# Optimization experiments

Measured on AMD Instinct MI355X. Metric: run time of the kernel, lower is better.

The kernel has to match this reference:

```python
import jax, jax.numpy as jnp
import numpy as np

N_NODES = 20000
N_EDGES = 320000
F_IN, HID, OUT = 128, 256, 32
N_LAYERS = 30
N_GRAPHS = 16


def setup_inputs() -> dict:
    key = jax.random.key(0)
    ks = jax.random.split(key, 10)
    x = jax.random.normal(ks[0], (N_NODES, F_IN), dtype=jnp.float32)
    edge_list = jax.random.randint(ks[1], (2, N_EDGES), 0, N_NODES, dtype=jnp.int64)
    batch = jnp.sort(jax.random.randint(ks[2], (N_NODES,), 0, N_GRAPHS, dtype=jnp.int64))
    # GCNConv weights: conv1, 29 middle layers, final linear
    W1 = jax.random.normal(ks[3], (F_IN, HID), dtype=jnp.float32) / np.sqrt(F_IN)
    b1 = jnp.zeros((HID,), dtype=jnp.float32)
    Wm = jax.random.normal(ks[4], (N_LAYERS - 1, HID, HID), dtype=jnp.float32) / np.sqrt(HID)
    bm = jnp.zeros((N_LAYERS - 1, HID), dtype=jnp.float32)
    Wlin = jax.random.normal(ks[5], (HID, OUT), dtype=jnp.float32) / np.sqrt(HID)
    blin = jnp.zeros((OUT,), dtype=jnp.float32)
    return {"x": x, "edge_list": edge_list, "batch": batch,
            "W1": W1, "b1": b1, "Wm": Wm, "bm": bm, "Wlin": Wlin, "blin": blin}


def reference(x, edge_list, batch, W1, b1, Wm, bm, Wlin, blin):
    n = x.shape[0]
    loop = jnp.arange(n, dtype=edge_list.dtype)
    src = jnp.concatenate([edge_list[0], loop])  # senders (+ self loops)
    dst = jnp.concatenate([edge_list[1], loop])  # receivers (+ self loops)
    # symmetric GCN normalization: deg counted at receivers incl. self loops
    deg = jax.ops.segment_sum(jnp.ones_like(dst, dtype=x.dtype), dst, num_segments=n)
    dinv = jnp.where(deg > 0, jax.lax.rsqrt(deg), 0.0)
    norm = dinv[src] * dinv[dst]  # [E+n]

    def conv(h, W, b):
        h = h @ W  # dense linear first (PyG GCNConv)
        agg = jax.ops.segment_sum(h[src] * norm[:, None], dst, num_segments=n)
        return jax.nn.relu(agg + b)

    h = conv(x, W1, b1)

    def step(h, wb):
        W, b = wb
        return conv(h, W, b), None

    h, _ = jax.lax.scan(step, h, (Wm, bm))

    # global mean pool over graphs
    counts = jax.ops.segment_sum(jnp.ones((n,), x.dtype), batch, num_segments=N_GRAPHS)
    pooled = jax.ops.segment_sum(h, batch, num_segments=N_GRAPHS) / jnp.maximum(counts, 1.0)[:, None]
    return pooled @ Wlin + blin
```

## Files before the change

kernel.cpp:

```cpp
#include <hip/hip_runtime.h>

typedef unsigned short u16;
typedef unsigned int u32;
typedef __attribute__((ext_vector_type(8))) _Float16 f16x8;
typedef __attribute__((ext_vector_type(4))) float f32x4;
typedef __attribute__((ext_vector_type(8))) u16 u16x8;

#define N_NODES 20000
#define N_EDGES 320000
#define F_IN 128
#define HID 256
#define OUT_F 32
#define N_LAYERS 30
#define N_GRAPHS 16
#define ELLCAP 64

__device__ __forceinline__ float h2f(u16 u) {
    _Float16 h;
    __builtin_memcpy(&h, &u, 2);
    return (float)h;
}
__device__ __forceinline__ u16 f2h(float f) {
    _Float16 h = (_Float16)f;
    u16 u;
    __builtin_memcpy(&u, &h, 2);
    return u;
}

__device__ __forceinline__ void gl_lds16(const u16* g, u16* l) {
    __builtin_amdgcn_global_load_lds((const u32*)g, (u32*)l, 16, 0, 0);
}

__global__ void fill_ell_kernel(const int* __restrict__ src, const int* __restrict__ dst,
                                int* __restrict__ cursor, u16* __restrict__ ell_col, int E) {
    int e = blockIdx.x * blockDim.x + threadIdx.x;
    if (e >= E) return;
    int s = src[e], d = dst[e];
    int slot = atomicAdd(&cursor[d], 1);
    if (slot < ELLCAP) ell_col[d * ELLCAP + slot] = (u16)s;
}

__global__ void dinv_kernel(const int* __restrict__ cnt, float* __restrict__ dinv, int n) {
    int i = blockIdx.x * blockDim.x + threadIdx.x;
    if (i < n) dinv[i] = rsqrtf((float)(cnt[i] + 1));
}

__global__ void prescale_x_kernel(const float* __restrict__ x, const int* __restrict__ cnt,
                                  u16* __restrict__ xs, int total) {
    int i = blockIdx.x * 256 + threadIdx.x;
    if (i < total) xs[i] = f2h(x[i] * rsqrtf((float)(cnt[i >> 7] + 1)));
}

__global__ __launch_bounds__(256) void transpose_f16_tiled(const float* __restrict__ W,
                                                           u16* __restrict__ T,
                                                           int K, int N) {
    __shared__ float tile[32][33];
    const int l = blockIdx.y;
    const int ntn = N >> 5;
    const int kt = blockIdx.x / ntn, ntile = blockIdx.x % ntn;
    const float* Wl = W + (size_t)l * K * N;
    u16* Tl = T + (size_t)l * K * N;
    const int r8 = threadIdx.x >> 5, c = threadIdx.x & 31;
    #pragma unroll
    for (int rr = 0; rr < 4; ++rr) {
        int r = rr * 8 + r8;
        tile[r][c] = Wl[(size_t)(kt * 32 + r) * N + ntile * 32 + c];
    }
    __syncthreads();
    #pragma unroll
    for (int rr = 0; rr < 4; ++rr) {
        int n = rr * 8 + r8;
        float v = tile[c][n];
        Tl[(size_t)(ntile * 32 + n) * K + kt * 32 + c] = f2h(v);
    }
}

template <int K>
__global__ __launch_bounds__(256, 3) void layer_fused(const u16* __restrict__ hs,
                                                      const u16* __restrict__ B,
                                                      const u16* __restrict__ ell_col,
                                                      const int* __restrict__ cnt,
                                                      const float* __restrict__ dinv,
                                                      const float* __restrict__ bias,
                                                      const float* __restrict__ rowscale,
                                                      u16* __restrict__ Ch,
                                                      float* __restrict__ C) {
    __shared__ u16 cols[32 * ELLCAP];
    __shared__ __align__(16) u16 gs[32 * HID];
    __shared__ __align__(16) u16 Bs[256 * 64];
    const int node0 = blockIdx.x * 32;
    const int tid = threadIdx.x;
    *(u16x8*)&cols[tid * 8] = *(const u16x8*)&ell_col[(size_t)node0 * ELLCAP + tid * 8];
    const int nd = tid >> 3, sub = tid & 7;
    const int node = node0 + nd;
    int c = cnt[node]; c = c < ELLCAP ? c : ELLCAP;
    const float dd = dinv[node];
    __syncthreads();
    const u16* cl = &cols[nd * ELLCAP];
    const int nb = (c + 7) >> 3;
    constexpr int S = K / 64;
    const int p0 = blockIdx.x & (S - 1);

    #pragma unroll 1
    for (int pi = 0; pi < S; ++pi) {
        const int p = (pi + p0) & (S - 1);
        const int f = p * 64 + sub * 8;
        f32x4 a0 = {}, a1 = {};
        {
            u16x8 sv = *(const u16x8*)(hs + (size_t)node * K + f);
            #pragma unroll
            for (int i = 0; i < 4; ++i) a0[i] += h2f(sv[i]);
            #pragma unroll
            for (int i = 0; i < 4; ++i) a1[i] += h2f(sv[i + 4]);
        }
        if (nb > 0) {
            u16x8 vbuf[8];
            u16x8 cc = *(const u16x8*)&cl[0];
            #pragma unroll
            for (int j = 0; j < 8; ++j) vbuf[j] = *(const u16x8*)(hs + (size_t)cc[j] * K + f);
            int base = 0;
            for (int b = 1; b < nb; ++b) {
                u16x8 cn = *(const u16x8*)&cl[b * 8];
                u16x8 vn[8];
                #pragma unroll
                for (int j = 0; j < 8; ++j) vn[j] = *(const u16x8*)(hs + (size_t)cn[j] * K + f);
                #pragma unroll
                for (int j = 0; j < 8; ++j) {
                    #pragma unroll
                    for (int i = 0; i < 4; ++i) a0[i] += h2f(vbuf[j][i]);
                    #pragma unroll
                    for (int i = 0; i < 4; ++i) a1[i] += h2f(vbuf[j][i + 4]);
                }
                base += 8;
                #pragma unroll
                for (int j = 0; j < 8; ++j) vbuf[j] = vn[j];
            }
            const u16x8 zz = {};
            #pragma unroll
            for (int j = 0; j < 8; ++j) {
                u16x8 v = (base + j < c) ? vbuf[j] : zz;
                #pragma unroll
                for (int i = 0; i < 4; ++i) a0[i] += h2f(v[i]);
                #pragma unroll
                for (int i = 0; i < 4; ++i) a1[i] += h2f(v[i + 4]);
            }
        }
        u16x8 o;
        #pragma unroll
        for (int i = 0; i < 4; ++i) o[i] = f2h(a0[i] * dd);
        #pragma unroll
        for (int i = 0; i < 4; ++i) o[i + 4] = f2h(a1[i] * dd);
        const int cc_ = p * 8 + sub;
        *(u16x8*)&gs[nd * K + ((cc_ ^ (nd & 7)) << 3)] = o;
    }

    const int wave = tid >> 6, lane = tid & 63;
    const int lr = lane >> 3, lc = lane & 7;
    #pragma unroll
    for (int q = 0; q < 8; ++q) {
        int rl = (wave * 8 + q) * 8 + lr;
        gl_lds16(B + (size_t)rl * K + ((lc ^ (rl & 7)) << 3), &Bs[(wave * 8 + q) * 512]);
    }
    f32x4 acc[2][4] = {};
    #pragma unroll
    for (int k = 0; k < S; ++k) {
        __syncthreads();
        const int k0 = k * 64;
        #pragma unroll
        for (int kk = 0; kk < 2; ++kk) {
            const int c8 = kk * 4 + (lane >> 4);
            f16x8 bf[4];
            #pragma unroll
            for (int nt = 0; nt < 4; ++nt) {
                int n = wave * 64 + nt * 16 + (lane & 15);
                bf[nt] = *(const f16x8*)&Bs[n * 64 + ((c8 ^ (n & 7)) << 3)];
            }
            #pragma unroll
            for (int mt = 0; mt < 2; ++mt) {
                int ml = mt * 16 + (lane & 15);
                int cg = (k0 >> 3) + c8;
                f16x8 af = *(const f16x8*)&gs[ml * K + ((cg ^ (ml & 7)) << 3)];
                #pragma unroll
                for (int nt = 0; nt < 4; ++nt)
                    acc[mt][nt] = __builtin_amdgcn_mfma_f32_16x16x32_f16(af, bf[nt], acc[mt][nt], 0, 0, 0);
            }
        }
        if (k + 1 < S) {
            __syncthreads();
            const int kn = k0 + 64;
            #pragma unroll
            for (int q = 0; q < 8; ++q) {
                int rl = (wave * 8 + q) * 8 + lr;
                gl_lds16(B + (size_t)rl * K + kn + ((lc ^ (rl & 7)) << 3), &Bs[(wave * 8 + q) * 512]);
            }
        }
    }
    __syncthreads();
    if (Ch) {
        #pragma unroll
        for (int mt = 0; mt < 2; ++mt) {
            #pragma unroll
            for (int r = 0; r < 4; ++r) {
                int lrow = mt * 16 + ((lane >> 4) << 2) + r;
                float sc = rowscale ? rowscale[node0 + lrow] : 1.f;
                #pragma unroll
                for (int nt = 0; nt < 4; ++nt) {
                    int gc = wave * 64 + nt * 16 + (lane & 15);
                    float v = sc * fmaxf(acc[mt][nt][r] + bias[gc], 0.f);
                    gs[lrow * HID + (gc ^ ((lrow & 7) << 3))] = f2h(v);
                }
            }
        }
        __syncthreads();
        const int row = tid >> 3, colb = (tid & 7) * 32;
        #pragma unroll
        for (int j = 0; j < 4; ++j) {
            int cs = (colb + j * 8) ^ ((row & 7) << 3);
            *(u16x8*)(Ch + (size_t)(node0 + row) * HID + colb + j * 8) = *(const u16x8*)&gs[row * HID + cs];
        }
    } else {
        float* Bf = (float*)Bs;
        #pragma unroll
        for (int mt = 0; mt < 2; ++mt) {
            #pragma unroll
            for (int r = 0; r < 4; ++r) {
                int lrow = mt * 16 + ((lane >> 4) << 2) + r;
                float sc = rowscale ? rowscale[node0 + lrow] : 1.f;
                #pragma unroll
                for (int nt = 0; nt < 4; ++nt) {
                    int gc = wave * 64 + nt * 16 + (lane & 15);
                    float v = sc * fmaxf(acc[mt][nt][r] + bias[gc], 0.f);
                    Bf[lrow * HID + (gc ^ ((lrow & 7) << 2))] = v;
                }
            }
        }
        __syncthreads();
        const int row = tid >> 3, colb = (tid & 7) * 32;
        #pragma unroll
        for (int j = 0; j < 8; ++j) {
            int cs = (colb + j * 4) ^ ((row & 7) << 2);
            *(f32x4*)(C + (size_t)(node0 + row) * HID + colb + j * 4) = *(const f32x4*)&Bf[row * HID + cs];
        }
    }
}

#define POOL_CHUNK 32
__global__ __launch_bounds__(256) void pool_kernel(const float* __restrict__ h,
                                                   const int* __restrict__ batch,
                                                   float* __restrict__ pool_sum) {
    int f = threadIdx.x;
    int start = blockIdx.x * POOL_CHUNK;
    int end = start + POOL_CHUNK; end = end < N_NODES ? end : N_NODES;
    if (start >= N_NODES) return;
    int gcur = batch[start];
    float acc = 0.f;
    for (int i = start; i < end; ++i) {
        int g = batch[i];
        if (g != gcur) { atomicAdd(&pool_sum[gcur * HID + f], acc); acc = 0.f; gcur = g; }
        acc += h[(size_t)i * HID + f];
    }
    atomicAdd(&pool_sum[gcur * HID + f], acc);
}

__device__ int lb_int(const int* __restrict__ a, int n, int v) {
    int lo = 0, hi = n;
    while (lo < hi) {
        int mid = (lo + hi) >> 1;
        if (a[mid] < v) lo = mid + 1; else hi = mid;
    }
    return lo;
}

__global__ void final_linear_kernel(const float* __restrict__ pool_sum,
                                    const int* __restrict__ batch,
                                    const float* __restrict__ Wlin,
                                    const float* __restrict__ blin,
                                    float* __restrict__ out) {
    int idx = blockIdx.x * blockDim.x + threadIdx.x;
    if (idx >= N_GRAPHS * OUT_F) return;
    int g = idx / OUT_F, o = idx % OUT_F;
    int lo = lb_int(batch, N_NODES, g);
    int hi = lb_int(batch, N_NODES, g + 1);
    float cinv = 1.f / fmaxf((float)(hi - lo), 1.f);
    float s = blin[o];
    for (int k = 0; k < HID; ++k) s += (pool_sum[g * HID + k] * cinv) * Wlin[k * OUT_F + o];
    out[idx] = s;
}

static inline size_t align_up(size_t x, size_t a) { return (x + a - 1) & ~(a - 1); }

extern "C" void kernel_launch(void* const* d_in, const int* in_sizes, int n_in,
                              void* d_out, int out_size, void* d_ws, size_t ws_size,
                              hipStream_t stream) {
    const float* x     = (const float*)d_in[0];
    const int*   elist = (const int*)d_in[1];
    const int*   batch = (const int*)d_in[2];
    const float* W1    = (const float*)d_in[3];
    const float* b1    = (const float*)d_in[4];
    const float* Wm    = (const float*)d_in[5];
    const float* bm    = (const float*)d_in[6];
    const float* Wlin  = (const float*)d_in[7];
    const float* blin  = (const float*)d_in[8];
    float* outp = (float*)d_out;

    const int* srcA = elist;
    const int* dstA = elist + N_EDGES;

    char* ws = (char*)d_ws;
    size_t off = 0;
    float* h      = (float*)(ws + off); off = align_up(off + sizeof(float) * N_NODES * HID, 1024);
    u16*   hA     = (u16*)(ws + off);   off = align_up(off + sizeof(u16) * N_NODES * HID, 1024);
    u16*   hB     = (u16*)(ws + off);   off = align_up(off + sizeof(u16) * N_NODES * HID, 1024);
    u16*   xs     = (u16*)(ws + off);   off = align_up(off + sizeof(u16) * N_NODES * F_IN, 1024);
    u16*   W1T    = (u16*)(ws + off);   off = align_up(off + sizeof(u16) * F_IN * HID, 1024);
    u16*   WmT    = (u16*)(ws + off);   off = align_up(off + sizeof(u16) * (N_LAYERS - 1) * HID * HID, 1024);
    int*   cursor = (int*)(ws + off);   off = align_up(off + sizeof(int) * N_NODES, 1024);
    float* dinv   = (float*)(ws + off); off = align_up(off + sizeof(float) * N_NODES, 1024);
    u16*   ell_col = (u16*)(ws + off);  off = align_up(off + sizeof(u16) * N_NODES * ELLCAP, 1024);
    float* pool_sum = (float*)(ws + off); off = align_up(off + sizeof(float) * N_GRAPHS * HID, 1024);

    hipMemsetAsync(cursor, 0, sizeof(int) * N_NODES, stream);
    hipMemsetAsync(ell_col, 0, sizeof(u16) * N_NODES * ELLCAP, stream);
    hipMemsetAsync(pool_sum, 0, sizeof(float) * N_GRAPHS * HID, stream);

    fill_ell_kernel<<<(N_EDGES + 255) / 256, 256, 0, stream>>>(srcA, dstA, cursor, ell_col, N_EDGES);
    dinv_kernel<<<(N_NODES + 255) / 256, 256, 0, stream>>>(cursor, dinv, N_NODES);
    prescale_x_kernel<<<(N_NODES * F_IN + 255) / 256, 256, 0, stream>>>(x, cursor, xs, N_NODES * F_IN);

    transpose_f16_tiled<<<dim3((F_IN / 32) * (HID / 32), 1), 256, 0, stream>>>(W1, W1T, F_IN, HID);
    transpose_f16_tiled<<<dim3((HID / 32) * (HID / 32), N_LAYERS - 1), 256, 0, stream>>>(Wm, WmT, HID, HID);

    const int lgrid = N_NODES / 32;
    layer_fused<F_IN><<<lgrid, 256, 0, stream>>>(xs, W1T, ell_col, cursor, dinv, b1, dinv, hA, h);
    u16* cur = hA; u16* nxt = hB;
    for (int l = 0; l < N_LAYERS - 1; ++l) {
        const bool last = (l == N_LAYERS - 2);
        layer_fused<HID><<<lgrid, 256, 0, stream>>>(cur, WmT + (size_t)l * HID * HID,
                                                    ell_col, cursor, dinv,
                                                    bm + (size_t)l * HID,
                                                    last ? nullptr : dinv,
                                                    last ? nullptr : nxt, h);
        u16* t = cur; cur = nxt; nxt = t;
    }
    pool_kernel<<<(N_NODES + POOL_CHUNK - 1) / POOL_CHUNK, 256, 0, stream>>>(h, batch, pool_sum);
    final_linear_kernel<<<2, 256, 0, stream>>>(pool_sum, batch, Wlin, blin, outp);
}
```

Before: 948.1 us.

## Read weight fragments directly from global memory instead of staging in LDS

Drops the LDS staging buffer for the weight matrix B and loads MFMA B-fragments straight from global memory, which is expected to hit L2 since every block reads the same weights. This removes the per-k-step barriers and the async global-to-LDS copies, and frees 32KB of LDS per block so more blocks can be resident. The fp32 output path also writes accumulators directly to global instead of transposing through LDS. The cost is uncoalesced 16-byte global reads repeated per block and scattered scalar fp32 stores.

```diff
diff --git a/kernel.cpp b/kernel.cpp
--- a/kernel.cpp
+++ b/kernel.cpp
@@ -25,10 +25,6 @@
     u16 u;
     __builtin_memcpy(&u, &h, 2);
     return u;
-}
-
-__device__ __forceinline__ void gl_lds16(const u16* g, u16* l) {
-    __builtin_amdgcn_global_load_lds((const u32*)g, (u32*)l, 16, 0, 0);
 }
 
 __global__ void fill_ell_kernel(const int* __restrict__ src, const int* __restrict__ dst,
@@ -87,7 +83,6 @@
                                                       float* __restrict__ C) {
     __shared__ u16 cols[32 * ELLCAP];
     __shared__ __align__(16) u16 gs[32 * HID];
-    __shared__ __align__(16) u16 Bs[256 * 64];
     const int node0 = blockIdx.x * 32;
     const int tid = threadIdx.x;
     *(u16x8*)&cols[tid * 8] = *(const u16x8*)&ell_col[(size_t)node0 * ELLCAP + tid * 8];
@@ -155,16 +150,10 @@
     }
 
     const int wave = tid >> 6, lane = tid & 63;
-    const int lr = lane >> 3, lc = lane & 7;
-    #pragma unroll
-    for (int q = 0; q < 8; ++q) {
-        int rl = (wave * 8 + q) * 8 + lr;
-        gl_lds16(B + (size_t)rl * K + ((lc ^ (rl & 7)) << 3), &Bs[(wave * 8 + q) * 512]);
-    }
     f32x4 acc[2][4] = {};
+    __syncthreads();
     #pragma unroll
     for (int k = 0; k < S; ++k) {
-        __syncthreads();
         const int k0 = k * 64;
         #pragma unroll
         for (int kk = 0; kk < 2; ++kk) {
@@ -173,7 +162,7 @@
             #pragma unroll
             for (int nt = 0; nt < 4; ++nt) {
                 int n = wave * 64 + nt * 16 + (lane & 15);
-                bf[nt] = *(const f16x8*)&Bs[n * 64 + ((c8 ^ (n & 7)) << 3)];
+                bf[nt] = *(const f16x8*)(B + (size_t)n * K + k0 + c8 * 8);
             }
             #pragma unroll
             for (int mt = 0; mt < 2; ++mt) {
@@ -185,18 +174,9 @@
                     acc[mt][nt] = __builtin_amdgcn_mfma_f32_16x16x32_f16(af, bf[nt], acc[mt][nt], 0, 0, 0);
             }
         }
-        if (k + 1 < S) {
-            __syncthreads();
-            const int kn = k0 + 64;
-            #pragma unroll
-            for (int q = 0; q < 8; ++q) {
-                int rl = (wave * 8 + q) * 8 + lr;
-                gl_lds16(B + (size_t)rl * K + kn + ((lc ^ (rl & 7)) << 3), &Bs[(wave * 8 + q) * 512]);
-            }
-        }
-    }
-    __syncthreads();
+    }
     if (Ch) {
+        __syncthreads();
         #pragma unroll
         for (int mt = 0; mt < 2; ++mt) {
             #pragma unroll
@@ -219,27 +199,18 @@
             *(u16x8*)(Ch + (size_t)(node0 + row) * HID + colb + j * 8) = *(const u16x8*)&gs[row * HID + cs];
         }
     } else {
-        float* Bf = (float*)Bs;
         #pragma unroll
         for (int mt = 0; mt < 2; ++mt) {
+            int gr = node0 + mt * 16 + ((lane >> 4) << 2);
             #pragma unroll
             for (int r = 0; r < 4; ++r) {
-                int lrow = mt * 16 + ((lane >> 4) << 2) + r;
-                float sc = rowscale ? rowscale[node0 + lrow] : 1.f;
+                float sc = rowscale ? rowscale[gr + r] : 1.f;
                 #pragma unroll
                 for (int nt = 0; nt < 4; ++nt) {
                     int gc = wave * 64 + nt * 16 + (lane & 15);
-                    float v = sc * fmaxf(acc[mt][nt][r] + bias[gc], 0.f);
-                    Bf[lrow * HID + (gc ^ ((lrow & 7) << 2))] = v;
+                    C[(size_t)(gr + r) * HID + gc] = sc * fmaxf(acc[mt][nt][r] + bias[gc], 0.f);
                 }
             }
-        }
-        __syncthreads();
-        const int row = tid >> 3, colb = (tid & 7) * 32;
-        #pragma unroll
-        for (int j = 0; j < 8; ++j) {
-            int cs = (colb + j * 4) ^ ((row & 7) << 2);
-            *(f32x4*)(C + (size_t)(node0 + row) * HID + colb + j * 4) = *(const f32x4*)&Bf[row * HID + cs];
         }
     }
 }
```

New measurement: 1.077 ms. 13.7% more time.

## Sort nodes by degree bucket so each block processes similar-degree rows

Applied to the files above, without the earlier changes.

Adds a counting sort of nodes by clamped in-degree (histogram, scan, scatter) and has each layer block gather its 32 nodes through a permutation. Output rows, row scales and neighbor lists are indexed by the permuted node ids. The goal is to cut load imbalance inside a block, where the whole block waits on the highest-degree node. The cost is a few small setup kernels plus scattered rather than contiguous row reads and writes, and the rotated per-block starting offset for the feature chunks is removed.

```diff
diff --git a/kernel.cpp b/kernel.cpp
--- a/kernel.cpp
+++ b/kernel.cpp
@@ -49,6 +49,26 @@
                                   u16* __restrict__ xs, int total) {
     int i = blockIdx.x * 256 + threadIdx.x;
     if (i < total) xs[i] = f2h(x[i] * rsqrtf((float)(cnt[i >> 7] + 1)));
+}
+
+__global__ void hist_kernel(const int* __restrict__ cnt, int* __restrict__ hist, int n) {
+    int i = blockIdx.x * blockDim.x + threadIdx.x;
+    if (i >= n) return;
+    int k = cnt[i]; k = k < ELLCAP ? k : ELLCAP;
+    atomicAdd(&hist[k], 1);
+}
+__global__ void scan_kernel(const int* __restrict__ hist, int* __restrict__ cur) {
+    if (threadIdx.x == 0) {
+        int s = 0;
+        for (int i = 0; i <= ELLCAP; ++i) { cur[i] = s; s += hist[i]; }
+    }
+}
+__global__ void scatter_kernel(const int* __restrict__ cnt, int* __restrict__ cur,
+                               int* __restrict__ perm, int n) {
+    int i = blockIdx.x * blockDim.x + threadIdx.x;
+    if (i >= n) return;
+    int k = cnt[i]; k = k < ELLCAP ? k : ELLCAP;
+    perm[atomicAdd(&cur[k], 1)] = i;
 }
 
 __global__ __launch_bounds__(256) void transpose_f16_tiled(const float* __restrict__ W,
@@ -83,27 +103,28 @@
                                                       const float* __restrict__ dinv,
                                                       const float* __restrict__ bias,
                                                       const float* __restrict__ rowscale,
+                                                      const int* __restrict__ perm,
                                                       u16* __restrict__ Ch,
                                                       float* __restrict__ C) {
     __shared__ u16 cols[32 * ELLCAP];
     __shared__ __align__(16) u16 gs[32 * HID];
     __shared__ __align__(16) u16 Bs[256 * 64];
+    __shared__ int pnode[32];
     const int node0 = blockIdx.x * 32;
     const int tid = threadIdx.x;
-    *(u16x8*)&cols[tid * 8] = *(const u16x8*)&ell_col[(size_t)node0 * ELLCAP + tid * 8];
     const int nd = tid >> 3, sub = tid & 7;
-    const int node = node0 + nd;
+    const int node = perm[node0 + nd];
+    if (sub == 0) pnode[nd] = node;
+    *(u16x8*)&cols[nd * ELLCAP + sub * 8] = *(const u16x8*)&ell_col[(size_t)node * ELLCAP + sub * 8];
     int c = cnt[node]; c = c < ELLCAP ? c : ELLCAP;
     const float dd = dinv[node];
     __syncthreads();
     const u16* cl = &cols[nd * ELLCAP];
     const int nb = (c + 7) >> 3;
     constexpr int S = K / 64;
-    const int p0 = blockIdx.x & (S - 1);
 
     #pragma unroll 1
-    for (int pi = 0; pi < S; ++pi) {
-        const int p = (pi + p0) & (S - 1);
+    for (int p = 0; p < S; ++p) {
         const int f = p * 64 + sub * 8;
         f32x4 a0 = {}, a1 = {};
         {
@@ -202,7 +223,7 @@
             #pragma unroll
             for (int r = 0; r < 4; ++r) {
                 int lrow = mt * 16 + ((lane >> 4) << 2) + r;
-                float sc = rowscale ? rowscale[node0 + lrow] : 1.f;
+                float sc = rowscale ? rowscale[pnode[lrow]] : 1.f;
                 #pragma unroll
                 for (int nt = 0; nt < 4; ++nt) {
                     int gc = wave * 64 + nt * 16 + (lane & 15);
@@ -213,10 +234,11 @@
         }
         __syncthreads();
         const int row = tid >> 3, colb = (tid & 7) * 32;
+        const size_t prow = (size_t)pnode[row];
         #pragma unroll
         for (int j = 0; j < 4; ++j) {
             int cs = (colb + j * 8) ^ ((row & 7) << 3);
-            *(u16x8*)(Ch + (size_t)(node0 + row) * HID + colb + j * 8) = *(const u16x8*)&gs[row * HID + cs];
+            *(u16x8*)(Ch + prow * HID + colb + j * 8) = *(const u16x8*)&gs[row * HID + cs];
         }
     } else {
         float* Bf = (float*)Bs;
@@ -225,7 +247,7 @@
             #pragma unroll
             for (int r = 0; r < 4; ++r) {
                 int lrow = mt * 16 + ((lane >> 4) << 2) + r;
-                float sc = rowscale ? rowscale[node0 + lrow] : 1.f;
+                float sc = rowscale ? rowscale[pnode[lrow]] : 1.f;
                 #pragma unroll
                 for (int nt = 0; nt < 4; ++nt) {
                     int gc = wave * 64 + nt * 16 + (lane & 15);
@@ -236,10 +258,11 @@
         }
         __syncthreads();
         const int row = tid >> 3, colb = (tid & 7) * 32;
+        const size_t prow = (size_t)pnode[row];
         #pragma unroll
         for (int j = 0; j < 8; ++j) {
             int cs = (colb + j * 4) ^ ((row & 7) << 2);
-            *(f32x4*)(C + (size_t)(node0 + row) * HID + colb + j * 4) = *(const f32x4*)&Bf[row * HID + cs];
+            *(f32x4*)(C + prow * HID + colb + j * 4) = *(const f32x4*)&Bf[row * HID + cs];
         }
     }
 }
@@ -318,27 +341,34 @@
     float* dinv   = (float*)(ws + off); off = align_up(off + sizeof(float) * N_NODES, 1024);
     u16*   ell_col = (u16*)(ws + off);  off = align_up(off + sizeof(u16) * N_NODES * ELLCAP, 1024);
     float* pool_sum = (float*)(ws + off); off = align_up(off + sizeof(float) * N_GRAPHS * HID, 1024);
+    int*   perm   = (int*)(ws + off);   off = align_up(off + sizeof(int) * N_NODES, 1024);
+    int*   hist   = (int*)(ws + off);   off = align_up(off + sizeof(int) * (ELLCAP + 1), 1024);
+    int*   buckcur = (int*)(ws + off);  off = align_up(off + sizeof(int) * (ELLCAP + 1), 1024);
 
     hipMemsetAsync(cursor, 0, sizeof(int) * N_NODES, stream);
     hipMemsetAsync(ell_col, 0, sizeof(u16) * N_NODES * ELLCAP, stream);
     hipMemsetAsync(pool_sum, 0, sizeof(float) * N_GRAPHS * HID, stream);
+    hipMemsetAsync(hist, 0, sizeof(int) * (ELLCAP + 1), stream);
 
     fill_ell_kernel<<<(N_EDGES + 255) / 256, 256, 0, stream>>>(srcA, dstA, cursor, ell_col, N_EDGES);
     dinv_kernel<<<(N_NODES + 255) / 256, 256, 0, stream>>>(cursor, dinv, N_NODES);
     prescale_x_kernel<<<(N_NODES * F_IN + 255) / 256, 256, 0, stream>>>(x, cursor, xs, N_NODES * F_IN);
+    hist_kernel<<<(N_NODES + 255) / 256, 256, 0, stream>>>(cursor, hist, N_NODES);
+    scan_kernel<<<1, 64, 0, stream>>>(hist, buckcur);
+    scatter_kernel<<<(N_NODES + 255) / 256, 256, 0, stream>>>(cursor, buckcur, perm, N_NODES);
 
     transpose_f16_tiled<<<dim3((F_IN / 32) * (HID / 32), 1), 256, 0, stream>>>(W1, W1T, F_IN, HID);
     transpose_f16_tiled<<<dim3((HID / 32) * (HID / 32), N_LAYERS - 1), 256, 0, stream>>>(Wm, WmT, HID, HID);
 
     const int lgrid = N_NODES / 32;
-    layer_fused<F_IN><<<lgrid, 256, 0, stream>>>(xs, W1T, ell_col, cursor, dinv, b1, dinv, hA, h);
+    layer_fused<F_IN><<<lgrid, 256, 0, stream>>>(xs, W1T, ell_col, cursor, dinv, b1, dinv, perm, hA, h);
     u16* cur = hA; u16* nxt = hB;
     for (int l = 0; l < N_LAYERS - 1; ++l) {
         const bool last = (l == N_LAYERS - 2);
         layer_fused<HID><<<lgrid, 256, 0, stream>>>(cur, WmT + (size_t)l * HID * HID,
                                                     ell_col, cursor, dinv,
                                                     bm + (size_t)l * HID,
-                                                    last ? nullptr : dinv,
+                                                    last ? nullptr : dinv, perm,
                                                     last ? nullptr : nxt, h);
         u16* t = cur; cur = nxt; nxt = t;
     }
```

New measurement: 1.079 ms. 1.14x slower.
